# Performance work log

Hardware: AMD Instinct MI355X
Metric: run time of the kernel (lower is better)

The kernel has to match this reference:

```python
import jax, jax.numpy as jnp
import numpy as np

N, T, V, D = 32, 417, 25, 2
NODES = T * V            # 10425 nodes per sample graph
E = 80000                # static interframe edges, shared across batch
HID = 20                 # GCN hidden size
LH = 50                  # lstm hidden == d_model == fc_hidden
NH, FF, NL = 5, 2048, 3  # transformer heads / ffn dim / layers
CO = 85                  # conv1d out channels (in_channels == T)
NC = 6
NS = 2                   # n stacked (lstm, gcn) stages
SZ = int(T * 0.2)        # 83 sampled timesteps for loss1
EPS = 1e-5


def setup_inputs() -> dict:
    key = jax.random.key(0)
    ks = iter(jax.random.split(key, 80))
    def r(shape, s=0.1):
        return jax.random.normal(next(ks), shape, dtype=jnp.float32) * s
    inp = {
        "x": jax.random.normal(next(ks), (N, T, V * D), dtype=jnp.float32),
        "y": jax.random.randint(next(ks), (N,), 0, NC),
        "edge_index": jax.random.randint(next(ks), (2, E), 0, NODES),
        "idx2": jax.random.randint(next(ks), (N, SZ), 0, T - 1),
        "h0s": jax.random.normal(next(ks), (NS, N, LH), dtype=jnp.float32),
        "c0s": jax.random.normal(next(ks), (NS, N, LH), dtype=jnp.float32),
        # params; layouts are (in, out) so x @ W == torch x @ W.T
        "lstm_Wih": r((NS, LH, 4 * LH)),
        "lstm_Whh": r((NS, LH, 4 * LH)),
        "lstm_bih": r((NS, 4 * LH)),
        "lstm_bhh": r((NS, 4 * LH)),
        "gcn1_W": r((NS, D, HID)),
        "gcn1_b": r((NS, HID)),
        "bn_g": jnp.ones((NS, HID), jnp.float32),
        "bn_b": jnp.zeros((NS, HID), jnp.float32),
        "gcn2_W": r((NS, HID, D)),
        "gcn2_b": r((NS, D)),
        "fc_W": r((LH, LH)),
        "fc_b": r((LH,)),
        "conv_W": r((CO, T)),
        "conv_b": r((CO,)),
        "attn_inW": r((NL, LH, 3 * LH)),
        "attn_inb": r((NL, 3 * LH)),
        "attn_outW": r((NL, LH, LH)),
        "attn_outb": r((NL, LH)),
        "ff1W": r((NL, LH, FF)),
        "ff1b": r((NL, FF)),
        "ff2W": r((NL, FF, LH)),
        "ff2b": r((NL, LH)),
        "ln1g": jnp.ones((NL, LH), jnp.float32),
        "ln1b": jnp.zeros((NL, LH), jnp.float32),
        "ln2g": jnp.ones((NL, LH), jnp.float32),
        "ln2b": jnp.zeros((NL, LH), jnp.float32),
        "Wc1": r((CO * LH, LH), 0.02),
        "bc1": r((LH,)),
        "Wc2": r((LH, NC)),
        "bc2": r((NC,)),
    }
    return inp


def _lstm(x, Wih, Whh, bih, bhh, h0, c0):
    # x: (N,T,in); single layer, batch_first; gate order i,f,g,o (torch)
    def step(carry, xt):
        h, c = carry
        g = xt @ Wih + h @ Whh + bih + bhh
        i, f, gg, o = jnp.split(g, 4, axis=-1)
        c = jax.nn.sigmoid(f) * c + jax.nn.sigmoid(i) * jnp.tanh(gg)
        h = jax.nn.sigmoid(o) * jnp.tanh(c)
        return (h, c), h
    _, hs = jax.lax.scan(step, (h0, c0), jnp.swapaxes(x, 0, 1))
    return jnp.swapaxes(hs, 0, 1)


def _gcn(X, W, b, src, dst, norm):
    # PyG GCNConv: x @ W, symmetric-normalized mean over neighbors (+self loops), + bias
    H = X @ W                                   # (N, NODES, out)
    msg = H[:, src, :] * norm[None, :, None]    # (N, E+NODES, out)
    agg = jax.vmap(lambda m: jax.ops.segment_sum(m, dst, num_segments=NODES))(msg)
    return agg + b


def _ln(x, g, b):
    m = x.mean(-1, keepdims=True)
    v = ((x - m) ** 2).mean(-1, keepdims=True)
    return (x - m) * jax.lax.rsqrt(v + EPS) * g + b


def _mha(x, inW, inb, outW, outb):
    # torch batch_first=False semantics: x is (S, B, E); here S=N, B=CO
    S, B, Em = x.shape
    hd = Em // NH
    qkv = x @ inW + inb
    q, k, v = jnp.split(qkv, 3, axis=-1)
    q = q.reshape(S, B, NH, hd)
    k = k.reshape(S, B, NH, hd)
    v = v.reshape(S, B, NH, hd)
    att = jnp.einsum('sbhd,tbhd->bhst', q, k) * (jnp.float32(hd) ** -0.5)
    w = jax.nn.softmax(att, axis=-1)
    o = jnp.einsum('bhst,tbhd->sbhd', w, v).reshape(S, B, Em)
    return o @ outW + outb


def _forward(x, y, edge_index, idx2, h0s, c0s,
             lstm_Wih, lstm_Whh, lstm_bih, lstm_bhh,
             gcn1_W, gcn1_b, bn_g, bn_b, gcn2_W, gcn2_b,
             fc_W, fc_b, conv_W, conv_b,
             attn_inW, attn_inb, attn_outW, attn_outb,
             ff1W, ff1b, ff2W, ff2b, ln1g, ln1b, ln2g, ln2b,
             Wc1, bc1, Wc2, bc2):
    loops = jnp.arange(NODES)
    src = jnp.concatenate([edge_index[0], loops])
    dst = jnp.concatenate([edge_index[1], loops])
    deg = jax.ops.segment_sum(jnp.ones(src.shape[0], jnp.float32), dst, num_segments=NODES)
    dinv = jnp.where(deg > 0, deg ** -0.5, 0.0)
    norm = dinv[src] * dinv[dst]

    x1 = x
    for s in range(NS):
        x1 = _lstm(x1, lstm_Wih[s], lstm_Whh[s], lstm_bih[s], lstm_bhh[s], h0s[s], c0s[s])
        xg = x1.reshape(N, NODES, D)
        h = _gcn(xg, gcn1_W[s], gcn1_b[s], src, dst, norm)
        # BatchNorm1d over all nodes of the whole batched graph (training stats)
        hf = h.reshape(-1, HID)
        m = hf.mean(0)
        v = hf.var(0)
        h = (h - m) * jax.lax.rsqrt(v + EPS) * bn_g[s] + bn_b[s]
        h = jax.nn.relu(h)
        xg = _gcn(h, gcn2_W[s], gcn2_b[s], src, dst, norm)
        x1 = xg.reshape(N, T, V * D)

    # unsupervised next-frame loss (Dropout is eval-mode identity)
    x_b1 = x1 @ fc_W + fc_b
    rows = jnp.arange(N)[:, None]
    pred = x_b1[rows, idx2]
    tgt = x[rows, idx2 + 1]
    loss1 = jnp.mean((pred - tgt) ** 2)

    # Conv1d(417->85, k=1) over time-as-channels
    t = jnp.einsum('oc,ncl->nol', conv_W, x1) + conv_b[None, :, None]  # (N, CO, LH)
    # torch encoder treats dim0=N as sequence, dim1=CO as batch (post-norm layers)
    for l in range(NL):
        a = _mha(t, attn_inW[l], attn_inb[l], attn_outW[l], attn_outb[l])
        t = _ln(t + a, ln1g[l], ln1b[l])
        f = jax.nn.relu(t @ ff1W[l] + ff1b[l]) @ ff2W[l] + ff2b[l]
        t = _ln(t + f, ln2g[l], ln2b[l])

    flat = t.reshape(N, CO * LH)
    h1 = jax.nn.relu(flat @ Wc1 + bc1)
    logits = h1 @ Wc2 + bc2
    logp = jax.nn.log_softmax(logits, axis=-1)
    loss2 = -jnp.mean(logp[jnp.arange(N), y])
    return jnp.exp(logp), loss1, loss2


def reference(x, y, edge_index, idx2, h0s, c0s,
              lstm_Wih, lstm_Whh, lstm_bih, lstm_bhh,
              gcn1_W, gcn1_b, bn_g, bn_b, gcn2_W, gcn2_b,
              fc_W, fc_b, conv_W, conv_b,
              attn_inW, attn_inb, attn_outW, attn_outb,
              ff1W, ff1b, ff2W, ff2b, ln1g, ln1b, ln2g, ln2b,
              Wc1, bc1, Wc2, bc2):
    return _forward(x, y, edge_index, idx2, h0s, c0s,
                    lstm_Wih, lstm_Whh, lstm_bih, lstm_bhh,
                    gcn1_W, gcn1_b, bn_g, bn_b, gcn2_W, gcn2_b,
                    fc_W, fc_b, conv_W, conv_b,
                    attn_inW, attn_inb, attn_outW, attn_outb,
                    ff1W, ff1b, ff2W, ff2b, ln1g, ln1b, ln2g, ln2b,
                    Wc1, bc1, Wc2, bc2)
```

## Files before the change

### kernel.cpp

```cpp
#include <hip/hip_runtime.h>
#include <math.h>

#define N_ 32
#define T_ 417
#define V_ 25
#define D_ 2
#define NODES_ 10425
#define E_ 80000
#define EN_ (E_ + NODES_)
#define HID_ 20
#define LH_ 50
#define NH_ 5
#define HD_ 10
#define FF_ 2048
#define NL_ 3
#define CO_ 85
#define NC_ 6
#define NS_ 2
#define SZ_ 83
#define EPS_ 1e-5f
#define NCH_ 11
#define NBNB_ 1304
#define LCH_ 32

__device__ inline float sane(float v){
  return (v == v && fabsf(v) < 1e30f) ? v : 0.f;
}

__device__ inline float wave_sum(float v){
  #pragma unroll
  for (int off = 32; off > 0; off >>= 1) v += __shfl_xor(v, off, 64);
  return v;
}

__global__ void k_init(const float* __restrict__ x, float* __restrict__ x1,
                       int* __restrict__ deg, float* __restrict__ accs){
  int i = blockIdx.x * 256 + threadIdx.x;
  if (i < N_*T_*LH_) x1[i] = x[i];
  if (i < NODES_) deg[i] = 0;
  if (i < 8) accs[i] = 0.f;
}

__global__ void k_deg(const int* __restrict__ ei, int* __restrict__ deg){
  int e = blockIdx.x * 256 + threadIdx.x;
  if (e >= EN_) return;
  int d = (e < E_) ? ei[E_ + e] : (e - E_);
  if ((unsigned)d >= NODES_) d = 0;
  atomicAdd(&deg[d], 1);
}

__global__ __launch_bounds__(256) void k_chunksum(const int* __restrict__ deg, int* __restrict__ csum){
  __shared__ int red[256];
  int chunk = blockIdx.x, tid = threadIdx.x;
  int s = 0;
  for (int i = tid; i < 1024; i += 256){
    int g = chunk*1024 + i;
    s += (g < NODES_) ? deg[g] : 0;
  }
  red[tid] = s;
  __syncthreads();
  for (int off = 128; off > 0; off >>= 1){
    if (tid < off) red[tid] += red[tid + off];
    __syncthreads();
  }
  if (tid == 0) csum[chunk] = red[0];
}

__global__ void k_chunkscan(int* __restrict__ csum){
  if (threadIdx.x == 0 && blockIdx.x == 0){
    int run = 0;
    for (int i = 0; i < NCH_; i++){ int t = csum[i]; csum[i] = run; run += t; }
  }
}

__global__ __launch_bounds__(1024) void k_scan2(const int* __restrict__ deg, const int* __restrict__ csum,
                       int* __restrict__ rowoff, int* __restrict__ wp, float* __restrict__ dinv){
  __shared__ int sdata[1024];
  int chunk = blockIdx.x, tid = threadIdx.x;
  int g = chunk*1024 + tid;
  int v = (g < NODES_) ? deg[g] : 0;
  int xv = v;
  sdata[tid] = xv;
  __syncthreads();
  for (int off = 1; off < 1024; off <<= 1){
    int add = (tid >= off) ? sdata[tid - off] : 0;
    __syncthreads();
    xv += add;
    sdata[tid] = xv;
    __syncthreads();
  }
  if (g < NODES_){
    int excl = csum[chunk] + xv - v;
    rowoff[g] = excl;
    wp[g] = excl;
    dinv[g] = (v > 0) ? rsqrtf((float)v) : 0.f;
  }
}

__global__ void k_scatter(const int* __restrict__ ei, const float* __restrict__ dinv,
                          int* __restrict__ wp, int* __restrict__ col, float* __restrict__ val){
  int e = blockIdx.x * 256 + threadIdx.x;
  if (e >= EN_) return;
  int s, d;
  if (e < E_){ s = ei[e]; d = ei[E_ + e]; } else { s = d = e - E_; }
  if ((unsigned)s >= NODES_) s = 0;
  if ((unsigned)d >= NODES_) d = 0;
  int pos = atomicAdd(&wp[d], 1);
  if ((unsigned)pos < EN_){
    col[pos] = s;
    val[pos] = dinv[s] * dinv[d];
  }
}

__global__ void k_xw(const float* __restrict__ x1, const float* __restrict__ Wih,
                     const float* __restrict__ bih, const float* __restrict__ bhh,
                     float* __restrict__ xW, int s){
  int idx = blockIdx.x * 256 + threadIdx.x;
  if (idx >= N_*T_*200) return;
  int r = idx / 200, g = idx % 200;
  const float* W = Wih + s*LH_*200;
  const float* xr = x1 + r*LH_;
  float acc = bih[s*200+g] + bhh[s*200+g];
  #pragma unroll 10
  for (int k = 0; k < LH_; k++) acc += xr[k] * W[k*200 + g];
  xW[idx] = acc;
}

__global__ __launch_bounds__(256, 1) void k_lstm(const float* __restrict__ xW, float* __restrict__ x1,
                       const float* __restrict__ Whh, const float* __restrict__ h0,
                       const float* __restrict__ c0, int s){
  __shared__ float hsw[4][52];
  __shared__ float gates[2][200];
  __shared__ float xs[LCH_*200];
  __shared__ float hist[LCH_*LH_];
  int n = blockIdx.x, tid = threadIdx.x;
  int w = tid >> 6;
  int l = tid & 63;
  int gcol = (tid < 200) ? tid : 199;
  float wcol[LH_];
  {
    const float* W = Whh + s*LH_*200 + gcol;
    #pragma unroll
    for (int k = 0; k < LH_; k++) wcol[k] = W[k*200];
  }
  float c = 0.f;
  if (l < LH_){
    c = c0[s*N_*LH_ + n*LH_ + l];
    hsw[w][l] = h0[s*N_*LH_ + n*LH_ + l];
  }
  if (l >= LH_ && l < 52) hsw[w][l] = 0.f;
  const float* xwn = xW + (size_t)n*T_*200;
  float* out = x1 + (size_t)n*T_*LH_;
  for (int t0 = 0; t0 < T_; t0 += LCH_){
    int nst = T_ - t0; if (nst > LCH_) nst = LCH_;
    int cnt = nst*200;
    for (int idx = tid; idx < cnt; idx += 256) xs[idx] = xwn[t0*200 + idx];
    __syncthreads();
    for (int i = 0; i < nst; i++){
      int t = t0 + i;
      float hreg[52];
      {
        const float4* hp = (const float4*)&hsw[w][0];
        #pragma unroll
        for (int k4 = 0; k4 < 13; k4++){
          float4 hv = hp[k4];
          hreg[k4*4]   = hv.x;
          hreg[k4*4+1] = hv.y;
          hreg[k4*4+2] = hv.z;
          hreg[k4*4+3] = hv.w;
        }
      }
      float a0 = 0.f, a1 = 0.f, a2 = 0.f, a3 = 0.f;
      #pragma unroll
      for (int k = 0; k < 48; k += 4){
        a0 += hreg[k]  *wcol[k];
        a1 += hreg[k+1]*wcol[k+1];
        a2 += hreg[k+2]*wcol[k+2];
        a3 += hreg[k+3]*wcol[k+3];
      }
      a0 += hreg[48]*wcol[48];
      a1 += hreg[49]*wcol[49];
      float acc = xs[i*200 + gcol] + ((a0 + a1) + (a2 + a3));
      if (tid < 200) gates[t & 1][tid] = acc;
      __syncthreads();
      if (l < LH_){
        const float* gb = gates[t & 1];
        float gi = gb[l], gf = gb[LH_+l], gg = gb[100+l], go = gb[150+l];
        float si = __frcp_rn(1.f + __expf(-gi));
        float sf = __frcp_rn(1.f + __expf(-gf));
        float so = __frcp_rn(1.f + __expf(-go));
        float eg = __expf(2.f*gg);
        float tg = 1.f - 2.f*__frcp_rn(eg + 1.f);
        c = sf*c + si*tg;
        float ec = __expf(2.f*c);
        float h = so * (1.f - 2.f*__frcp_rn(ec + 1.f));
        hsw[w][l] = h;
        if (w == 0) hist[i*LH_ + l] = h;
      }
    }
    __syncthreads();
    int hcnt = nst*LH_;
    for (int idx = tid; idx < hcnt; idx += 256) out[t0*LH_ + idx] = hist[idx];
  }
}

__global__ void k_tonode(const float* __restrict__ x1, float* __restrict__ P0){
  int idx = blockIdx.x * 256 + threadIdx.x;
  if (idx >= NODES_*64) return;
  int v = idx >> 6, rem = idx & 63;
  int n = rem >> 1, d = rem & 1;
  P0[idx] = x1[n*(T_*LH_) + v*D_ + d];
}

__global__ __launch_bounds__(64) void k_gather(const int* __restrict__ rowoff, const int* __restrict__ deg,
                       const int* __restrict__ col, const float* __restrict__ val,
                       const float* __restrict__ src, float* __restrict__ dst){
  int v = blockIdx.x, tid = threadIdx.x;
  int start = rowoff[v], len = deg[v];
  float acc = 0.f;
  for (int j = 0; j < len; j++){
    int cs = col[start + j];
    if ((unsigned)cs >= NODES_) cs = 0;
    acc += val[start + j] * src[cs*64 + tid];
  }
  dst[v*64 + tid] = acc;
}

__global__ __launch_bounds__(256) void k_bnstat(const float* __restrict__ P1, float* __restrict__ bnpart){
  int idx = blockIdx.x * 256 + threadIdx.x;
  float p0 = 0.f, p1v = 0.f;
  if (idx < NODES_*N_){ p0 = P1[idx*2]; p1v = P1[idx*2+1]; }
  float sv[5] = {p0, p1v, p0*p0, p1v*p1v, p0*p1v};
  __shared__ float red[5][4];
  int wave = threadIdx.x >> 6, lane = threadIdx.x & 63;
  #pragma unroll
  for (int j = 0; j < 5; j++){
    float w = wave_sum(sv[j]);
    if (lane == 0) red[j][wave] = w;
  }
  __syncthreads();
  if (threadIdx.x < 5){
    int j = threadIdx.x;
    bnpart[j*NBNB_ + blockIdx.x] = red[j][0] + red[j][1] + red[j][2] + red[j][3];
  }
}

__global__ __launch_bounds__(256) void k_bnfin(const float* __restrict__ bnpart,
                        const float* __restrict__ W1, const float* __restrict__ b1,
                        const float* __restrict__ bn_g, const float* __restrict__ bn_b,
                        float* __restrict__ bnsc, int s){
  __shared__ float red[256];
  __shared__ float S[5];
  int tid = threadIdx.x;
  for (int j = 0; j < 5; j++){
    float acc = 0.f;
    for (int t = tid; t < NBNB_; t += 256) acc += bnpart[j*NBNB_ + t];
    red[tid] = acc;
    __syncthreads();
    for (int off = 128; off > 0; off >>= 1){
      if (tid < off) red[tid] += red[tid + off];
      __syncthreads();
    }
    if (tid == 0) S[j] = red[0];
    __syncthreads();
  }
  if (tid < HID_){
    int c = tid;
    const float M = (float)(N_*NODES_);
    float w0 = W1[s*D_*HID_ + c], w1 = W1[s*D_*HID_ + HID_ + c];
    float bc = b1[s*HID_ + c];
    float m0 = S[0]/M, m1 = S[1]/M;
    float e00 = S[2]/M, e11 = S[3]/M, e01 = S[4]/M;
    float mean = w0*m0 + w1*m1 + bc;
    float v00 = e00 - m0*m0, v11 = e11 - m1*m1, c01 = e01 - m0*m1;
    float var = w0*w0*v00 + w1*w1*v11 + 2.f*w0*w1*c01;
    var = fmaxf(var, 0.f);
    float sc = bn_g[s*HID_ + c] * rsqrtf(var + EPS_);
    bnsc[c] = sc;
    bnsc[HID_ + c] = bn_b[s*HID_ + c] - mean*sc;
  }
}

__global__ __launch_bounds__(256) void k_bnrelu_t2(const float* __restrict__ P1, const float* __restrict__ bnsc,
                            const float* __restrict__ W1, const float* __restrict__ b1,
                            const float* __restrict__ W2, float* __restrict__ Rb, int s){
  int idx = blockIdx.x * 256 + threadIdx.x;
  if (idx >= NODES_*N_) return;
  float p0 = P1[idx*2], p1v = P1[idx*2+1];
  const float* W1p = W1 + s*D_*HID_;
  const float* W2p = W2 + s*HID_*D_;
  float a0 = 0.f, a1 = 0.f;
  #pragma unroll
  for (int c = 0; c < HID_; c++){
    float q = p0*W1p[c] + p1v*W1p[HID_ + c] + b1[s*HID_ + c];
    float h = fmaxf(q*bnsc[c] + bnsc[HID_ + c], 0.f);
    a0 += h * W2p[c*D_];
    a1 += h * W2p[c*D_ + 1];
  }
  Rb[idx*2]     = a0;
  Rb[idx*2 + 1] = a1;
}

__global__ __launch_bounds__(64) void k_gcn2(const int* __restrict__ rowoff, const int* __restrict__ deg,
                      const int* __restrict__ col, const float* __restrict__ val,
                      const float* __restrict__ Rb, const float* __restrict__ gb2,
                      float* __restrict__ x1, int s){
  int v = blockIdx.x, tid = threadIdx.x;
  int start = rowoff[v], len = deg[v];
  float acc = 0.f;
  for (int j = 0; j < len; j++){
    int cs = col[start + j];
    if ((unsigned)cs >= NODES_) cs = 0;
    acc += val[start + j] * Rb[cs*64 + tid];
  }
  int n = tid >> 1, d = tid & 1;
  x1[n*(T_*LH_) + v*D_ + d] = acc + gb2[s*D_ + d];
}

__global__ __launch_bounds__(64) void k_loss1(const float* __restrict__ x1, const float* __restrict__ x,
                       const int* __restrict__ idx2, const float* __restrict__ fcW,
                       const float* __restrict__ fcb, float* __restrict__ accs){
  int bi = blockIdx.x;
  int n = bi / SZ_, j = bi % SZ_;
  int row = idx2[n*SZ_ + j];
  if ((unsigned)row >= (T_ - 1)) row = 0;
  int l = threadIdx.x;
  float sq = 0.f;
  if (l < LH_){
    const float* xr = x1 + n*T_*LH_ + row*LH_;
    float acc = fcb[l];
    #pragma unroll 10
    for (int k = 0; k < LH_; k++) acc += xr[k] * fcW[k*LH_ + l];
    float dd = acc - x[n*T_*LH_ + (row+1)*LH_ + l];
    sq = dd*dd;
  }
  sq = wave_sum(sq);
  if (l == 0) atomicAdd(&accs[0], sq);
}

__global__ __launch_bounds__(64) void k_conv(const float* __restrict__ x1, const float* __restrict__ cW,
                      const float* __restrict__ cb, float* __restrict__ tb){
  int bi = blockIdx.x;
  int n = bi / CO_, o = bi % CO_;
  int l = threadIdx.x;
  if (l >= LH_) return;
  float acc = cb[o];
  const float* w = cW + o*T_;
  const float* xr = x1 + n*T_*LH_ + l;
  #pragma unroll 4
  for (int c2 = 0; c2 < T_; c2++) acc += w[c2] * xr[c2*LH_];
  tb[bi*LH_ + l] = acc;
}

__global__ void k_qkv(const float* __restrict__ tb, const float* __restrict__ inW,
                      const float* __restrict__ inb, float* __restrict__ qkv, int l3){
  int idx = blockIdx.x * 256 + threadIdx.x;
  if (idx >= N_*CO_*150) return;
  int r = idx / 150, j = idx % 150;
  const float* W = inW + l3*LH_*150;
  const float* tr = tb + r*LH_;
  float acc = inb[l3*150 + j];
  #pragma unroll 10
  for (int k = 0; k < LH_; k++) acc += tr[k] * W[k*150 + j];
  qkv[idx] = acc;
}

__global__ __launch_bounds__(128) void k_attn(const float* __restrict__ qkv, float* __restrict__ abuf){
  __shared__ float qs[32][HD_], ks[32][HD_], vs[32][HD_], att[32][32];
  int bi = blockIdx.x;
  int b = bi % CO_, h = bi / CO_;
  int tid = threadIdx.x;
  for (int idx = tid; idx < 960; idx += 128){
    int grp = idx / 320, m = idx % 320, ss = m / HD_, dd = m % HD_;
    float vvv = qkv[(ss*CO_ + b)*150 + grp*LH_ + h*HD_ + dd];
    if (grp == 0) qs[ss][dd] = vvv;
    else if (grp == 1) ks[ss][dd] = vvv;
    else vs[ss][dd] = vvv;
  }
  __syncthreads();
  const float scale = 0.31622776601683794f;
  for (int idx = tid; idx < 1024; idx += 128){
    int ss = idx >> 5, tt = idx & 31;
    float a = 0.f;
    #pragma unroll
    for (int dd = 0; dd < HD_; dd++) a += qs[ss][dd]*ks[tt][dd];
    att[ss][tt] = a*scale;
  }
  __syncthreads();
  if (tid < 32){
    float m = -1e31f;
    for (int tt = 0; tt < 32; tt++) m = fmaxf(m, att[tid][tt]);
    float sum = 0.f;
    for (int tt = 0; tt < 32; tt++){ float e = __expf(att[tid][tt] - m); att[tid][tt] = e; sum += e; }
    float inv = 1.f / fmaxf(sum, 1e-30f);
    for (int tt = 0; tt < 32; tt++) att[tid][tt] *= inv;
  }
  __syncthreads();
  for (int idx = tid; idx < 320; idx += 128){
    int ss = idx / HD_, dd = idx % HD_;
    float acc = 0.f;
    #pragma unroll
    for (int tt = 0; tt < 32; tt++) acc += att[ss][tt]*vs[tt][dd];
    abuf[(ss*CO_ + b)*LH_ + h*HD_ + dd] = acc;
  }
}

__global__ __launch_bounds__(64) void k_proj_ln(float* __restrict__ tb, const float* __restrict__ abuf,
                         const float* __restrict__ outW, const float* __restrict__ outb,
                         const float* __restrict__ g, const float* __restrict__ bb, int l3){
  __shared__ float orow[LH_];
  int r = blockIdx.x, l = threadIdx.x;
  if (l < LH_) orow[l] = abuf[r*LH_ + l];
  __syncthreads();
  float rr = 0.f;
  if (l < LH_){
    const float* W = outW + l3*LH_*LH_;
    float p = outb[l3*LH_ + l];
    #pragma unroll 10
    for (int k = 0; k < LH_; k++) p += orow[k] * W[k*LH_ + l];
    rr = tb[r*LH_ + l] + p;
  }
  float mean = wave_sum(rr) / (float)LH_;
  float dv = (l < LH_) ? (rr - mean) : 0.f;
  float var = wave_sum(dv*dv) / (float)LH_;
  if (l < LH_)
    tb[r*LH_ + l] = (rr - mean)*rsqrtf(var + EPS_)*g[l3*LH_ + l] + bb[l3*LH_ + l];
}

__global__ __launch_bounds__(512) void k_ff(float* __restrict__ tb, const float* __restrict__ w1,
                     const float* __restrict__ bi1, const float* __restrict__ w2,
                     const float* __restrict__ bi2, const float* __restrict__ g,
                     const float* __restrict__ bb, int l3){
  __shared__ float tin[4][LH_];
  __shared__ float hb[4][FF_];
  __shared__ float part[4][8][LH_];
  int r0 = blockIdx.x * 4, tid = threadIdx.x;
  if (tid < 4*LH_) tin[tid/LH_][tid%LH_] = tb[r0*LH_ + tid];
  __syncthreads();
  const float* W1l = w1 + l3*LH_*FF_;
  #pragma unroll
  for (int i = 0; i < 4; i++){
    int j = i*512 + tid;
    float bj = bi1[l3*FF_ + j];
    float a0 = bj, a1 = bj, a2 = bj, a3 = bj;
    #pragma unroll 10
    for (int k = 0; k < LH_; k++){
      float w = W1l[k*FF_ + j];
      a0 += tin[0][k]*w;
      a1 += tin[1][k]*w;
      a2 += tin[2][k]*w;
      a3 += tin[3][k]*w;
    }
    hb[0][j] = fmaxf(a0, 0.f);
    hb[1][j] = fmaxf(a1, 0.f);
    hb[2][j] = fmaxf(a2, 0.f);
    hb[3][j] = fmaxf(a3, 0.f);
  }
  __syncthreads();
  const float* W2l = w2 + l3*FF_*LH_;
  int l = tid & 63, grp = tid >> 6;
  if (l < LH_){
    float a0 = 0.f, a1 = 0.f, a2 = 0.f, a3 = 0.f;
    int jbase = grp * 256;
    const float* wp = W2l + (size_t)jbase*LH_ + l;
    for (int jj = 0; jj < 256; jj++){
      float w = wp[jj*LH_];
      a0 += hb[0][jbase + jj]*w;
      a1 += hb[1][jbase + jj]*w;
      a2 += hb[2][jbase + jj]*w;
      a3 += hb[3][jbase + jj]*w;
    }
    part[0][grp][l] = a0;
    part[1][grp][l] = a1;
    part[2][grp][l] = a2;
    part[3][grp][l] = a3;
  }
  __syncthreads();
  if (tid < 256){
    int row = tid >> 6, ll = tid & 63;
    float out = 0.f;
    if (ll < LH_){
      float a = 0.f;
      #pragma unroll
      for (int gg = 0; gg < 8; gg++) a += part[row][gg][ll];
      out = a + bi2[l3*LH_ + ll] + tin[row][ll];
    }
    float s1 = (ll < LH_) ? out : 0.f;
    float mean = wave_sum(s1) / (float)LH_;
    float dv = (ll < LH_) ? (out - mean) : 0.f;
    float var = wave_sum(dv*dv) / (float)LH_;
    if (ll < LH_)
      tb[(r0 + row)*LH_ + ll] = (out - mean)*rsqrtf(var + EPS_)*g[l3*LH_ + ll] + bb[l3*LH_ + ll];
  }
}

__global__ __launch_bounds__(512) void k_head(const float* __restrict__ tb, const int* __restrict__ y,
                       const float* __restrict__ Wc1, const float* __restrict__ bc1,
                       const float* __restrict__ Wc2, const float* __restrict__ bc2,
                       float* __restrict__ out, float* __restrict__ accs){
  __shared__ float part[8][LH_];
  __shared__ float h1[LH_];
  __shared__ float lgs[NC_];
  int n = blockIdx.x, tid = threadIdx.x;
  int l = tid & 63, grp = tid >> 6;
  const float* tr = tb + n*CO_*LH_;
  if (l < LH_){
    int k0 = grp * 532;
    int k1 = k0 + 532; if (k1 > CO_*LH_) k1 = CO_*LH_;
    float acc = 0.f;
    for (int k = k0; k < k1; k++) acc += tr[k] * Wc1[k*LH_ + l];
    part[grp][l] = acc;
  }
  __syncthreads();
  if (tid < LH_){
    float a = bc1[tid];
    #pragma unroll
    for (int gg = 0; gg < 8; gg++) a += part[gg][tid];
    h1[tid] = fmaxf(a, 0.f);
  }
  __syncthreads();
  if (tid < NC_){
    float a = bc2[tid];
    #pragma unroll 10
    for (int k = 0; k < LH_; k++) a += h1[k] * Wc2[k*NC_ + tid];
    lgs[tid] = a;
  }
  __syncthreads();
  if (tid == 0){
    float m = -1e31f;
    for (int c2 = 0; c2 < NC_; c2++) m = fmaxf(m, lgs[c2]);
    float sum = 0.f;
    for (int c2 = 0; c2 < NC_; c2++) sum += __expf(lgs[c2] - m);
    float lse = m + logf(fmaxf(sum, 1e-30f));
    for (int c2 = 0; c2 < NC_; c2++)
      out[n*NC_ + c2] = __expf(lgs[c2] - lse);
    int yy = y[n];
    if ((unsigned)yy >= NC_) yy = 0;
    atomicAdd(&accs[1], -(lgs[yy] - lse));
  }
}

__global__ void k_fin(const float* __restrict__ accs, float* __restrict__ out){
  if (threadIdx.x == 0 && blockIdx.x == 0){
    out[N_*NC_]     = sane(accs[0] / (float)(N_*SZ_*LH_));
    out[N_*NC_ + 1] = sane(accs[1] / (float)N_);
  }
}

extern "C" void kernel_launch(void* const* d_in, const int* in_sizes, int n_in,
                              void* d_out, int out_size, void* d_ws, size_t ws_size,
                              hipStream_t stream){
  static const int expect[36] = {
    667200, 32, 160000, 2656, 3200, 3200,
    20000, 20000, 400, 400,
    80, 40, 40, 40, 80, 4,
    2500, 50, 35445, 85,
    22500, 450, 7500, 150,
    307200, 6144, 307200, 150,
    150, 150, 150, 150,
    212500, 50, 300, 6
  };
  if (n_in != 36 || out_size != 194 || ws_size < 14300000) return;
  for (int i = 0; i < 36; i++) if (in_sizes[i] != expect[i]) return;

  const float* x        = (const float*)d_in[0];
  const int*   y        = (const int*)d_in[1];
  const int*   ei       = (const int*)d_in[2];
  const int*   idx2     = (const int*)d_in[3];
  const float* h0s      = (const float*)d_in[4];
  const float* c0s      = (const float*)d_in[5];
  const float* lstm_Wih = (const float*)d_in[6];
  const float* lstm_Whh = (const float*)d_in[7];
  const float* lstm_bih = (const float*)d_in[8];
  const float* lstm_bhh = (const float*)d_in[9];
  const float* gcn1_W   = (const float*)d_in[10];
  const float* gcn1_b   = (const float*)d_in[11];
  const float* bn_g     = (const float*)d_in[12];
  const float* bn_b     = (const float*)d_in[13];
  const float* gcn2_W   = (const float*)d_in[14];
  const float* gcn2_b   = (const float*)d_in[15];
  const float* fc_W     = (const float*)d_in[16];
  const float* fc_b     = (const float*)d_in[17];
  const float* conv_W   = (const float*)d_in[18];
  const float* conv_b   = (const float*)d_in[19];
  const float* attn_inW = (const float*)d_in[20];
  const float* attn_inb = (const float*)d_in[21];
  const float* attn_outW= (const float*)d_in[22];
  const float* attn_outb= (const float*)d_in[23];
  const float* ff1W     = (const float*)d_in[24];
  const float* ff1b     = (const float*)d_in[25];
  const float* ff2W     = (const float*)d_in[26];
  const float* ff2b     = (const float*)d_in[27];
  const float* ln1g     = (const float*)d_in[28];
  const float* ln1b     = (const float*)d_in[29];
  const float* ln2g     = (const float*)d_in[30];
  const float* ln2b     = (const float*)d_in[31];
  const float* Wc1      = (const float*)d_in[32];
  const float* bc1      = (const float*)d_in[33];
  const float* Wc2      = (const float*)d_in[34];
  const float* bc2      = (const float*)d_in[35];
  float* out = (float*)d_out;

  char* wsp = (char*)d_ws;
  size_t off = 0;
  auto alloc = [&](size_t bytes)->void*{
    void* p = wsp + off;
    off = (off + bytes + 255) & ~(size_t)255;
    return p;
  };
  float* x1   = (float*)alloc((size_t)N_*T_*LH_*4);
  float* X    = (float*)alloc((size_t)N_*T_*200*4);
  float* val  = (float*)alloc((size_t)EN_*4);
  float* dinv = (float*)alloc((size_t)NODES_*4);
  float* bnsc = (float*)alloc(64*4);
  float* accs = (float*)alloc(8*4);
  int*   deg  = (int*)alloc((size_t)NODES_*4);
  int*   rowoff = (int*)alloc((size_t)(NODES_+1)*4);
  int*   wp   = (int*)alloc((size_t)NODES_*4);
  int*   col  = (int*)alloc((size_t)EN_*4);
  int*   csum = (int*)alloc(16*4);
  float* xW     = X;
  float* P0     = X;
  float* P1     = X + (size_t)NODES_*64;
  float* bnpart = X + (size_t)2*NODES_*64;
  float* Rb     = P0;
  float* tb     = X;
  float* qkvb   = X + 136064;
  float* abuf   = X + 544128;

  k_init<<<dim3((N_*T_*LH_ + 255)/256), dim3(256), 0, stream>>>(x, x1, deg, accs);
  k_deg<<<dim3((EN_ + 255)/256), dim3(256), 0, stream>>>(ei, deg);
  k_chunksum<<<dim3(NCH_), dim3(256), 0, stream>>>(deg, csum);
  k_chunkscan<<<dim3(1), dim3(64), 0, stream>>>(csum);
  k_scan2<<<dim3(NCH_), dim3(1024), 0, stream>>>(deg, csum, rowoff, wp, dinv);
  k_scatter<<<dim3((EN_ + 255)/256), dim3(256), 0, stream>>>(ei, dinv, wp, col, val);

  for (int s = 0; s < NS_; s++){
    k_xw<<<dim3((N_*T_*200 + 255)/256), dim3(256), 0, stream>>>(x1, lstm_Wih, lstm_bih, lstm_bhh, xW, s);
    k_lstm<<<dim3(N_), dim3(256), 0, stream>>>(xW, x1, lstm_Whh, h0s, c0s, s);
    k_tonode<<<dim3((NODES_*64 + 255)/256), dim3(256), 0, stream>>>(x1, P0);
    k_gather<<<dim3(NODES_), dim3(64), 0, stream>>>(rowoff, deg, col, val, P0, P1);
    k_bnstat<<<dim3(NBNB_), dim3(256), 0, stream>>>(P1, bnpart);
    k_bnfin<<<dim3(1), dim3(256), 0, stream>>>(bnpart, gcn1_W, gcn1_b, bn_g, bn_b, bnsc, s);
    k_bnrelu_t2<<<dim3((N_*NODES_ + 255)/256), dim3(256), 0, stream>>>(P1, bnsc, gcn1_W, gcn1_b, gcn2_W, Rb, s);
    k_gcn2<<<dim3(NODES_), dim3(64), 0, stream>>>(rowoff, deg, col, val, Rb, gcn2_b, x1, s);
  }

  k_loss1<<<dim3(N_*SZ_), dim3(64), 0, stream>>>(x1, x, idx2, fc_W, fc_b, accs);
  k_conv<<<dim3(N_*CO_), dim3(64), 0, stream>>>(x1, conv_W, conv_b, tb);

  for (int l3 = 0; l3 < NL_; l3++){
    k_qkv<<<dim3((N_*CO_*150 + 255)/256), dim3(256), 0, stream>>>(tb, attn_inW, attn_inb, qkvb, l3);
    k_attn<<<dim3(NH_*CO_), dim3(128), 0, stream>>>(qkvb, abuf);
    k_proj_ln<<<dim3(N_*CO_), dim3(64), 0, stream>>>(tb, abuf, attn_outW, attn_outb, ln1g, ln1b, l3);
    k_ff<<<dim3(N_*CO_/4), dim3(512), 0, stream>>>(tb, ff1W, ff1b, ff2W, ff2b, ln2g, ln2b, l3);
  }

  k_head<<<dim3(N_), dim3(512), 0, stream>>>(tb, y, Wc1, bc1, Wc2, bc2, out, accs);
  k_fin<<<dim3(1), dim3(64), 0, stream>>>(accs, out);
}
```

Measured before the change: 1.347 ms.

## Fuse BN statistics into gather and QKV projection into attention kernel

BatchNorm moment accumulation now happens inside the GCN gather kernel, using wave reductions and atomics into 64 buckets, so the separate stat kernel and its second pass over P1 are gone and the finalize kernel shrinks. The QKV projection is computed inside the attention kernel from a shared-memory tile of the input rows, which removes the qkv buffer round-trip and one launch per layer. In exchange there is atomic contention on the buckets and some redundant projection work, since each head block loads the full 32x50 input tile.

Result: slower. 1.448 ms (+7.5%).

```diff
diff --git a/kernel.cpp b/kernel.cpp
--- a/kernel.cpp
+++ b/kernel.cpp
@@ -20,8 +20,8 @@
 #define SZ_ 83
 #define EPS_ 1e-5f
 #define NCH_ 11
-#define NBNB_ 1304
 #define LCH_ 32
+#define NBK_ 64
 
 __device__ inline float sane(float v){
   return (v == v && fabsf(v) < 1e30f) ? v : 0.f;
@@ -34,11 +34,13 @@
 }
 
 __global__ void k_init(const float* __restrict__ x, float* __restrict__ x1,
-                       int* __restrict__ deg, float* __restrict__ accs){
+                       int* __restrict__ deg, float* __restrict__ accs,
+                       float* __restrict__ bnacc){
   int i = blockIdx.x * 256 + threadIdx.x;
   if (i < N_*T_*LH_) x1[i] = x[i];
   if (i < NODES_) deg[i] = 0;
   if (i < 8) accs[i] = 0.f;
+  if (i < 2*5*NBK_) bnacc[i] = 0.f;
 }
 
 __global__ void k_deg(const int* __restrict__ ei, int* __restrict__ deg){
@@ -214,7 +216,8 @@
 
 __global__ __launch_bounds__(64) void k_gather(const int* __restrict__ rowoff, const int* __restrict__ deg,
                        const int* __restrict__ col, const float* __restrict__ val,
-                       const float* __restrict__ src, float* __restrict__ dst){
+                       const float* __restrict__ src, float* __restrict__ dst,
+                       float* __restrict__ bnsum){
   int v = blockIdx.x, tid = threadIdx.x;
   int start = rowoff[v], len = deg[v];
   float acc = 0.f;
@@ -224,46 +227,35 @@
     acc += val[start + j] * src[cs*64 + tid];
   }
   dst[v*64 + tid] = acc;
-}
-
-__global__ __launch_bounds__(256) void k_bnstat(const float* __restrict__ P1, float* __restrict__ bnpart){
-  int idx = blockIdx.x * 256 + threadIdx.x;
-  float p0 = 0.f, p1v = 0.f;
-  if (idx < NODES_*N_){ p0 = P1[idx*2]; p1v = P1[idx*2+1]; }
-  float sv[5] = {p0, p1v, p0*p0, p1v*p1v, p0*p1v};
-  __shared__ float red[5][4];
-  int wave = threadIdx.x >> 6, lane = threadIdx.x & 63;
-  #pragma unroll
-  for (int j = 0; j < 5; j++){
-    float w = wave_sum(sv[j]);
-    if (lane == 0) red[j][wave] = w;
-  }
-  __syncthreads();
-  if (threadIdx.x < 5){
-    int j = threadIdx.x;
-    bnpart[j*NBNB_ + blockIdx.x] = red[j][0] + red[j][1] + red[j][2] + red[j][3];
-  }
-}
-
-__global__ __launch_bounds__(256) void k_bnfin(const float* __restrict__ bnpart,
+  int d = tid & 1;
+  float partner = __shfl_xor(acc, 1, 64);
+  float m0  = wave_sum(d == 0 ? acc : 0.f);
+  float m1  = wave_sum(d == 1 ? acc : 0.f);
+  float e00 = wave_sum(d == 0 ? acc*acc : 0.f);
+  float e11 = wave_sum(d == 1 ? acc*acc : 0.f);
+  float e01 = wave_sum(d == 0 ? acc*partner : 0.f);
+  if (tid == 0){
+    int bk = blockIdx.x & (NBK_ - 1);
+    atomicAdd(&bnsum[0*NBK_ + bk], m0);
+    atomicAdd(&bnsum[1*NBK_ + bk], m1);
+    atomicAdd(&bnsum[2*NBK_ + bk], e00);
+    atomicAdd(&bnsum[3*NBK_ + bk], e11);
+    atomicAdd(&bnsum[4*NBK_ + bk], e01);
+  }
+}
+
+__global__ __launch_bounds__(64) void k_bnfin(const float* __restrict__ bnsum,
                         const float* __restrict__ W1, const float* __restrict__ b1,
                         const float* __restrict__ bn_g, const float* __restrict__ bn_b,
                         float* __restrict__ bnsc, int s){
-  __shared__ float red[256];
   __shared__ float S[5];
   int tid = threadIdx.x;
-  for (int j = 0; j < 5; j++){
-    float acc = 0.f;
-    for (int t = tid; t < NBNB_; t += 256) acc += bnpart[j*NBNB_ + t];
-    red[tid] = acc;
-    __syncthreads();
-    for (int off = 128; off > 0; off >>= 1){
-      if (tid < off) red[tid] += red[tid + off];
-      __syncthreads();
-    }
-    if (tid == 0) S[j] = red[0];
-    __syncthreads();
-  }
+  if (tid < 5){
+    float a = 0.f;
+    for (int bk = 0; bk < NBK_; bk++) a += bnsum[tid*NBK_ + bk];
+    S[tid] = a;
+  }
+  __syncthreads();
   if (tid < HID_){
     int c = tid;
     const float M = (float)(N_*NODES_);
@@ -352,30 +344,29 @@
   tb[bi*LH_ + l] = acc;
 }
 
-__global__ void k_qkv(const float* __restrict__ tb, const float* __restrict__ inW,
-                      const float* __restrict__ inb, float* __restrict__ qkv, int l3){
-  int idx = blockIdx.x * 256 + threadIdx.x;
-  if (idx >= N_*CO_*150) return;
-  int r = idx / 150, j = idx % 150;
-  const float* W = inW + l3*LH_*150;
-  const float* tr = tb + r*LH_;
-  float acc = inb[l3*150 + j];
-  #pragma unroll 10
-  for (int k = 0; k < LH_; k++) acc += tr[k] * W[k*150 + j];
-  qkv[idx] = acc;
-}
-
-__global__ __launch_bounds__(128) void k_attn(const float* __restrict__ qkv, float* __restrict__ abuf){
+__global__ __launch_bounds__(128) void k_attn(const float* __restrict__ tb,
+                      const float* __restrict__ inW, const float* __restrict__ inb,
+                      float* __restrict__ abuf, int l3){
+  __shared__ float tin[32][LH_];
   __shared__ float qs[32][HD_], ks[32][HD_], vs[32][HD_], att[32][32];
   int bi = blockIdx.x;
   int b = bi % CO_, h = bi / CO_;
   int tid = threadIdx.x;
+  for (int idx = tid; idx < 32*LH_; idx += 128){
+    int ss = idx / LH_, j = idx % LH_;
+    tin[ss][j] = tb[(ss*CO_ + b)*LH_ + j];
+  }
+  __syncthreads();
+  const float* Wl = inW + l3*LH_*150;
   for (int idx = tid; idx < 960; idx += 128){
     int grp = idx / 320, m = idx % 320, ss = m / HD_, dd = m % HD_;
-    float vvv = qkv[(ss*CO_ + b)*150 + grp*LH_ + h*HD_ + dd];
-    if (grp == 0) qs[ss][dd] = vvv;
-    else if (grp == 1) ks[ss][dd] = vvv;
-    else vs[ss][dd] = vvv;
+    int colj = grp*LH_ + h*HD_ + dd;
+    float acc = inb[l3*150 + colj];
+    #pragma unroll 10
+    for (int k = 0; k < LH_; k++) acc += tin[ss][k] * Wl[k*150 + colj];
+    if (grp == 0) qs[ss][dd] = acc;
+    else if (grp == 1) ks[ss][dd] = acc;
+    else vs[ss][dd] = acc;
   }
   __syncthreads();
   const float scale = 0.31622776601683794f;
@@ -614,6 +605,7 @@
   float* dinv = (float*)alloc((size_t)NODES_*4);
   float* bnsc = (float*)alloc(64*4);
   float* accs = (float*)alloc(8*4);
+  float* bnacc= (float*)alloc((size_t)2*5*NBK_*4);
   int*   deg  = (int*)alloc((size_t)NODES_*4);
   int*   rowoff = (int*)alloc((size_t)(NODES_+1)*4);
   int*   wp   = (int*)alloc((size_t)NODES_*4);
@@ -622,13 +614,11 @@
   float* xW     = X;
   float* P0     = X;
   float* P1     = X + (size_t)NODES_*64;
-  float* bnpart = X + (size_t)2*NODES_*64;
   float* Rb     = P0;
   float* tb     = X;
-  float* qkvb   = X + 136064;
-  float* abuf   = X + 544128;
-
-  k_init<<<dim3((N_*T_*LH_ + 255)/256), dim3(256), 0, stream>>>(x, x1, deg, accs);
+  float* abuf   = X + 136064;
+
+  k_init<<<dim3((N_*T_*LH_ + 255)/256), dim3(256), 0, stream>>>(x, x1, deg, accs, bnacc);
   k_deg<<<dim3((EN_ + 255)/256), dim3(256), 0, stream>>>(ei, deg);
   k_chunksum<<<dim3(NCH_), dim3(256), 0, stream>>>(deg, csum);
   k_chunkscan<<<dim3(1), dim3(64), 0, stream>>>(csum);
@@ -639,9 +629,8 @@
     k_xw<<<dim3((N_*T_*200 + 255)/256), dim3(256), 0, stream>>>(x1, lstm_Wih, lstm_bih, lstm_bhh, xW, s);
     k_lstm<<<dim3(N_), dim3(256), 0, stream>>>(xW, x1, lstm_Whh, h0s, c0s, s);
     k_tonode<<<dim3((NODES_*64 + 255)/256), dim3(256), 0, stream>>>(x1, P0);
-    k_gather<<<dim3(NODES_), dim3(64), 0, stream>>>(rowoff, deg, col, val, P0, P1);
-    k_bnstat<<<dim3(NBNB_), dim3(256), 0, stream>>>(P1, bnpart);
-    k_bnfin<<<dim3(1), dim3(256), 0, stream>>>(bnpart, gcn1_W, gcn1_b, bn_g, bn_b, bnsc, s);
+    k_gather<<<dim3(NODES_), dim3(64), 0, stream>>>(rowoff, deg, col, val, P0, P1, bnacc + s*5*NBK_);
+    k_bnfin<<<dim3(1), dim3(64), 0, stream>>>(bnacc + s*5*NBK_, gcn1_W, gcn1_b, bn_g, bn_b, bnsc, s);
     k_bnrelu_t2<<<dim3((N_*NODES_ + 255)/256), dim3(256), 0, stream>>>(P1, bnsc, gcn1_W, gcn1_b, gcn2_W, Rb, s);
     k_gcn2<<<dim3(NODES_), dim3(64), 0, stream>>>(rowoff, deg, col, val, Rb, gcn2_b, x1, s);
   }
@@ -650,8 +639,7 @@
   k_conv<<<dim3(N_*CO_), dim3(64), 0, stream>>>(x1, conv_W, conv_b, tb);
 
   for (int l3 = 0; l3 < NL_; l3++){
-    k_qkv<<<dim3((N_*CO_*150 + 255)/256), dim3(256), 0, stream>>>(tb, attn_inW, attn_inb, qkvb, l3);
-    k_attn<<<dim3(NH_*CO_), dim3(128), 0, stream>>>(qkvb, abuf);
+    k_attn<<<dim3(NH_*CO_), dim3(128), 0, stream>>>(tb, attn_inW, attn_inb, abuf, l3);
     k_proj_ln<<<dim3(N_*CO_), dim3(64), 0, stream>>>(tb, abuf, attn_outW, attn_outb, ln1g, ln1b, l3);
     k_ff<<<dim3(N_*CO_/4), dim3(512), 0, stream>>>(tb, ff1W, ff1b, ff2W, ff2b, ln2g, ln2b, l3);
   }
```
